# Performance work log

Hardware: AMD Instinct MI355X
Metric: run time of the kernel (lower is better)

Reference implementation:

```python
import jax, jax.numpy as jnp
import numpy as np

B, T, I, H, O = 1024, 512, 1, 64, 1


def _lstm_layer(x, Wih, Whh, bih, bhh):
    # x: [B,T,in]; Wih: [4H,in]; Whh: [4H,H]; biases: [4H]
    # Precompute input contribution for all timesteps (PyTorch adds both biases).
    xg = jnp.einsum('bti,gi->btg', x, Wih) + bih + bhh  # [B,T,4H]
    h0 = jnp.zeros((x.shape[0], H), x.dtype)

    def step(carry, xg_t):
        h, c = carry
        gates = xg_t + h @ Whh.T  # [B,4H], torch gate order i,f,g,o
        i, f, g, o = jnp.split(gates, 4, axis=-1)
        c = jax.nn.sigmoid(f) * c + jax.nn.sigmoid(i) * jnp.tanh(g)
        h = jax.nn.sigmoid(o) * jnp.tanh(c)
        return (h, c), h

    (_, _), hs = jax.lax.scan(step, (h0, h0), jnp.swapaxes(xg, 0, 1))
    return jnp.swapaxes(hs, 0, 1)  # [B,T,H]


def setup_inputs() -> dict:
    key = jax.random.key(0)
    ks = jax.random.split(key, 12)
    s = 1.0 / np.sqrt(H)  # torch LSTM/Linear init scale
    u = lambda k, shp: jax.random.uniform(k, shp, jnp.float32, -s, s)
    return {
        'x': jax.random.normal(ks[0], (B, T, I), jnp.float32),
        'W_ih0': u(ks[1], (4 * H, I)), 'W_hh0': u(ks[2], (4 * H, H)),
        'b_ih0': u(ks[3], (4 * H,)), 'b_hh0': u(ks[4], (4 * H,)),
        'W_ih1': u(ks[5], (4 * H, H)), 'W_hh1': u(ks[6], (4 * H, H)),
        'b_ih1': u(ks[7], (4 * H,)), 'b_hh1': u(ks[8], (4 * H,)),
        'W_fc': u(ks[9], (O, H)), 'b_fc': u(ks[10], (O,)),
    }


def reference(x, W_ih0, W_hh0, b_ih0, b_hh0, W_ih1, W_hh1, b_ih1, b_hh1, W_fc, b_fc):
    h1 = _lstm_layer(x, W_ih0, W_hh0, b_ih0, b_hh0)   # layer 0
    h2 = _lstm_layer(h1, W_ih1, W_hh1, b_ih1, b_hh1)  # layer 1
    return h2[:, -1, :] @ W_fc.T + b_fc  # [B,O]
```

## Files before the change

### kernel.cpp

```cpp
#include <hip/hip_runtime.h>

#define BB 1024
#define TT 512
#define HH 64
#define NB 4
#define NTHR 512

typedef _Float16 half8 __attribute__((ext_vector_type(8)));
typedef float f32x4 __attribute__((ext_vector_type(4)));

#if defined(__has_builtin)
#  if __has_builtin(__builtin_amdgcn_rcpf)
#    define FRCP(v) __builtin_amdgcn_rcpf(v)
#  endif
#endif
#ifndef FRCP
#  define FRCP(v) (1.0f / (v))
#endif

#define MFMA16(A, B, C) __builtin_amdgcn_mfma_f32_16x16x32_f16((A), (B), (C), 0, 0, 0)

__device__ __forceinline__ float fsig(float v) {
    return FRCP(1.0f + __expf(-v));
}
__device__ __forceinline__ float ftanh(float v) {
    return fmaf(2.0f, fsig(2.0f * v), -1.0f);
}

__device__ __forceinline__ half8 load_frag(const float* __restrict__ W, int row, int k0) {
    const float4* p = (const float4*)(W + row * HH + k0);
    float4 u = p[0], v = p[1];
    half8 r;
    r[0] = (_Float16)u.x; r[1] = (_Float16)u.y; r[2] = (_Float16)u.z; r[3] = (_Float16)u.w;
    r[4] = (_Float16)v.x; r[5] = (_Float16)v.y; r[6] = (_Float16)v.z; r[7] = (_Float16)v.w;
    return r;
}

__global__ __launch_bounds__(NTHR, 2)
void lstm_mfma2(const float* __restrict__ x,
                const float* __restrict__ Wih0,
                const float* __restrict__ Whh0,
                const float* __restrict__ bih0,
                const float* __restrict__ bhh0,
                const float* __restrict__ Wih1,
                const float* __restrict__ Whh1,
                const float* __restrict__ bih1,
                const float* __restrict__ bhh1,
                const float* __restrict__ Wfc,
                const float* __restrict__ bfc,
                float* __restrict__ out)
{
    __shared__ float s_x[NB][TT + 1];
    __shared__ __align__(16) _Float16 s_h0b[2][NB][80];
    __shared__ __align__(16) _Float16 s_h1b[2][NB][80];

    const int t    = threadIdx.x;
    const int lane = t & 63;
    const int w    = t >> 6;
    const int b0   = blockIdx.x * NB;

    const int arow = lane & 15;
    const int g4   = lane >> 4;
    const int bsrc = lane & 3;

    const int rep   = (lane >> 2) & 3;
    const int layer = rep >> 1;
    const int dd    = rep & 1;
    const int u     = 8 * w + 4 * dd + g4;

    half8 a0[2][2], a1i[2][2], a1h[2][2];
#pragma unroll
    for (int d = 0; d < 2; ++d) {
        const int row = (arow & 3) * 64 + 8 * w + 4 * d + (arow >> 2);
#pragma unroll
        for (int kk = 0; kk < 2; ++kk) {
            const int k0 = kk * 32 + g4 * 8;
            a0[d][kk]  = load_frag(Whh0, row, k0);
            a1i[d][kk] = load_frag(Wih1, row, k0);
            a1h[d][kk] = load_frag(Whh1, row, k0);
        }
    }

    f32x4 cb0[2], cb1[2];
#pragma unroll
    for (int d = 0; d < 2; ++d) {
        const int uu = 8 * w + 4 * d + g4;
#pragma unroll
        for (int q = 0; q < 4; ++q) {
            const int r = q * 64 + uu;
            cb0[d][q] = bih0[r] + bhh0[r];
            cb1[d][q] = bih1[r] + bhh1[r];
        }
    }
    float xw[4];
#pragma unroll
    for (int q = 0; q < 4; ++q) {
        xw[q] = (layer == 0) ? Wih0[q * 64 + u] : 0.0f;
    }

#pragma unroll
    for (int k = 0; k < (NB * TT) / NTHR; ++k) {
        int idx = t + NTHR * k;
        int nb  = idx >> 9;
        int pos = idx & (TT - 1);
        s_x[nb][pos] = x[(b0 + nb) * TT + pos];
    }
    {
        _Float16* z0 = &s_h0b[0][0][0];
        _Float16* z1 = &s_h1b[0][0][0];
        for (int i = t; i < 2 * NB * 80; i += NTHR) {
            z0[i] = (_Float16)0.0f;
            z1[i] = (_Float16)0.0f;
        }
    }

    float cst = 0.0f;
    __syncthreads();

    for (int s = 0; s <= TT; ++s) {
        const int rb = s & 1;
        const int wb = rb ^ 1;
        const int xs = (s < TT) ? s : (TT - 1);
        const float xv = s_x[bsrc][xs];

        const _Float16* h0p = &s_h0b[rb][bsrc][g4 * 8];
        const _Float16* h1p = &s_h1b[rb][bsrc][g4 * 8];
        half8 bh0_0 = *(const half8*)(h0p);
        half8 bh0_1 = *(const half8*)(h0p + 32);
        half8 bh1_0 = *(const half8*)(h1p);
        half8 bh1_1 = *(const half8*)(h1p + 32);

        f32x4 c0_0 = cb0[0], c0_1 = cb0[1];
        c0_0 = MFMA16(a0[0][0], bh0_0, c0_0);
        c0_1 = MFMA16(a0[1][0], bh0_0, c0_1);
        c0_0 = MFMA16(a0[0][1], bh0_1, c0_0);
        c0_1 = MFMA16(a0[1][1], bh0_1, c0_1);
        f32x4 c1a0 = cb1[0], c1a1 = cb1[1];
        f32x4 c1b0 = {0.f, 0.f, 0.f, 0.f}, c1b1 = {0.f, 0.f, 0.f, 0.f};
        c1a0 = MFMA16(a1i[0][0], bh0_0, c1a0);
        c1a1 = MFMA16(a1i[1][0], bh0_0, c1a1);
        c1b0 = MFMA16(a1h[0][0], bh1_0, c1b0);
        c1b1 = MFMA16(a1h[1][0], bh1_0, c1b1);
        c1a0 = MFMA16(a1i[0][1], bh0_1, c1a0);
        c1a1 = MFMA16(a1i[1][1], bh0_1, c1a1);
        c1b0 = MFMA16(a1h[0][1], bh1_1, c1b0);
        c1b1 = MFMA16(a1h[1][1], bh1_1, c1b1);
        f32x4 c1_0 = c1a0 + c1b0;
        f32x4 c1_1 = c1a1 + c1b1;

        f32x4 t0 = dd ? c0_1 : c0_0;
        f32x4 t1 = dd ? c1_1 : c1_0;
        f32x4 gv = layer ? t1 : t0;

        float gi = fmaf(xw[0], xv, gv[0]);
        float gf = fmaf(xw[1], xv, gv[1]);
        float gg = fmaf(xw[2], xv, gv[2]);
        float go = fmaf(xw[3], xv, gv[3]);

        const bool active = layer ? (s >= 1) : (s < TT);
        if (active) {
            float i_ = fsig(gi);
            float f_ = fsig(gf);
            float g_ = ftanh(gg);
            float o_ = fsig(go);
            cst = fmaf(f_, cst, i_ * g_);
            float hn = o_ * ftanh(cst);
            _Float16* dst = layer ? &s_h1b[wb][bsrc][u] : &s_h0b[wb][bsrc][u];
            *dst = (_Float16)hn;
        }
        __syncthreads();
    }

    if (t < NB * HH) {
        const int nb = t >> 6;
        const int j  = t & 63;
        float v = (float)s_h1b[1][nb][j] * Wfc[j];
#pragma unroll
        for (int off = 32; off > 0; off >>= 1) {
            v += __shfl_down(v, off);
        }
        if (j == 0) out[b0 + nb] = v + bfc[0];
    }
}

extern "C" void kernel_launch(void* const* d_in, const int* in_sizes, int n_in,
                              void* d_out, int out_size, void* d_ws, size_t ws_size,
                              hipStream_t stream) {
    const float* x    = (const float*)d_in[0];
    const float* Wih0 = (const float*)d_in[1];
    const float* Whh0 = (const float*)d_in[2];
    const float* bih0 = (const float*)d_in[3];
    const float* bhh0 = (const float*)d_in[4];
    const float* Wih1 = (const float*)d_in[5];
    const float* Whh1 = (const float*)d_in[6];
    const float* bih1 = (const float*)d_in[7];
    const float* bhh1 = (const float*)d_in[8];
    const float* Wfc  = (const float*)d_in[9];
    const float* bfc  = (const float*)d_in[10];
    float* out = (float*)d_out;

    lstm_mfma2<<<dim3(BB / NB), dim3(NTHR), 0, stream>>>(
        x, Wih0, Whh0, bih0, bhh0, Wih1, Whh1, bih1, bhh1, Wfc, bfc, out);
}
```

Measured before the change: 317.7 us.

## Halve batch per block and use four waves each covering 16 hidden units

Each block now handles 2 batch rows with 4 waves instead of 4 rows with 8 waves, so each wave owns 16 hidden units and issues 4 MFMA tiles per gate group. Lane mapping changes so each lane picks its gate value from 8 replicas (layer × dtile) over 2 batch sources. The launch has twice as many blocks, and each per-step barrier syncs only 4 waves, which is meant to cut barrier cost and raise parallelism across CUs. In exchange each wave does twice the MFMA work, holds twice the weight registers, and does more redundant selection work. The h buffers are padded to 96 halves.

```diff
diff --git a/kernel.cpp b/kernel.cpp
--- a/kernel.cpp
+++ b/kernel.cpp
@@ -3,8 +3,9 @@
 #define BB 1024
 #define TT 512
 #define HH 64
-#define NB 4
-#define NTHR 512
+#define NB 2
+#define NTHR 256
+#define HPAD 96
 
 typedef _Float16 half8 __attribute__((ext_vector_type(8)));
 typedef float f32x4 __attribute__((ext_vector_type(4)));
@@ -37,7 +38,7 @@
 }
 
 __global__ __launch_bounds__(NTHR, 2)
-void lstm_mfma2(const float* __restrict__ x,
+void lstm_mfma3(const float* __restrict__ x,
                 const float* __restrict__ Wih0,
                 const float* __restrict__ Whh0,
                 const float* __restrict__ bih0,
@@ -51,8 +52,8 @@
                 float* __restrict__ out)
 {
     __shared__ float s_x[NB][TT + 1];
-    __shared__ __align__(16) _Float16 s_h0b[2][NB][80];
-    __shared__ __align__(16) _Float16 s_h1b[2][NB][80];
+    __shared__ __align__(16) _Float16 s_h0b[2][NB][HPAD];
+    __shared__ __align__(16) _Float16 s_h1b[2][NB][HPAD];
 
     const int t    = threadIdx.x;
     const int lane = t & 63;
@@ -61,17 +62,16 @@
 
     const int arow = lane & 15;
     const int g4   = lane >> 4;
-    const int bsrc = lane & 3;
-
-    const int rep   = (lane >> 2) & 3;
-    const int layer = rep >> 1;
-    const int dd    = rep & 1;
-    const int u     = 8 * w + 4 * dd + g4;
-
-    half8 a0[2][2], a1i[2][2], a1h[2][2];
-#pragma unroll
-    for (int d = 0; d < 2; ++d) {
-        const int row = (arow & 3) * 64 + 8 * w + 4 * d + (arow >> 2);
+    const int bsrc = lane & 1;
+    const int rep   = (lane >> 1) & 7;
+    const int layer = rep & 1;
+    const int dtile = rep >> 1;
+    const int u     = 16 * w + 4 * dtile + g4;
+
+    half8 a0[4][2], a1i[4][2], a1h[4][2];
+#pragma unroll
+    for (int d = 0; d < 4; ++d) {
+        const int row = (arow & 3) * 64 + 16 * w + 4 * d + (arow >> 2);
 #pragma unroll
         for (int kk = 0; kk < 2; ++kk) {
             const int k0 = kk * 32 + g4 * 8;
@@ -81,10 +81,10 @@
         }
     }
 
-    f32x4 cb0[2], cb1[2];
-#pragma unroll
-    for (int d = 0; d < 2; ++d) {
-        const int uu = 8 * w + 4 * d + g4;
+    f32x4 cb0[4], cb1[4];
+#pragma unroll
+    for (int d = 0; d < 4; ++d) {
+        const int uu = 16 * w + 4 * d + g4;
 #pragma unroll
         for (int q = 0; q < 4; ++q) {
             const int r = q * 64 + uu;
@@ -108,7 +108,7 @@
     {
         _Float16* z0 = &s_h0b[0][0][0];
         _Float16* z1 = &s_h1b[0][0][0];
-        for (int i = t; i < 2 * NB * 80; i += NTHR) {
+        for (int i = t; i < 2 * NB * HPAD; i += NTHR) {
             z0[i] = (_Float16)0.0f;
             z1[i] = (_Float16)0.0f;
         }
@@ -130,26 +130,32 @@
         half8 bh1_0 = *(const half8*)(h1p);
         half8 bh1_1 = *(const half8*)(h1p + 32);
 
-        f32x4 c0_0 = cb0[0], c0_1 = cb0[1];
-        c0_0 = MFMA16(a0[0][0], bh0_0, c0_0);
-        c0_1 = MFMA16(a0[1][0], bh0_0, c0_1);
-        c0_0 = MFMA16(a0[0][1], bh0_1, c0_0);
-        c0_1 = MFMA16(a0[1][1], bh0_1, c0_1);
-        f32x4 c1a0 = cb1[0], c1a1 = cb1[1];
-        f32x4 c1b0 = {0.f, 0.f, 0.f, 0.f}, c1b1 = {0.f, 0.f, 0.f, 0.f};
-        c1a0 = MFMA16(a1i[0][0], bh0_0, c1a0);
-        c1a1 = MFMA16(a1i[1][0], bh0_0, c1a1);
-        c1b0 = MFMA16(a1h[0][0], bh1_0, c1b0);
-        c1b1 = MFMA16(a1h[1][0], bh1_0, c1b1);
-        c1a0 = MFMA16(a1i[0][1], bh0_1, c1a0);
-        c1a1 = MFMA16(a1i[1][1], bh0_1, c1a1);
-        c1b0 = MFMA16(a1h[0][1], bh1_1, c1b0);
-        c1b1 = MFMA16(a1h[1][1], bh1_1, c1b1);
-        f32x4 c1_0 = c1a0 + c1b0;
-        f32x4 c1_1 = c1a1 + c1b1;
-
-        f32x4 t0 = dd ? c0_1 : c0_0;
-        f32x4 t1 = dd ? c1_1 : c1_0;
+        f32x4 c0[4], c1[4];
+#pragma unroll
+        for (int d = 0; d < 4; ++d) c0[d] = cb0[d];
+#pragma unroll
+        for (int d = 0; d < 4; ++d) c0[d] = MFMA16(a0[d][0], bh0_0, c0[d]);
+#pragma unroll
+        for (int d = 0; d < 4; ++d) c0[d] = MFMA16(a0[d][1], bh0_1, c0[d]);
+#pragma unroll
+        for (int d = 0; d < 4; ++d) c1[d] = cb1[d];
+#pragma unroll
+        for (int d = 0; d < 4; ++d) c1[d] = MFMA16(a1i[d][0], bh0_0, c1[d]);
+#pragma unroll
+        for (int d = 0; d < 4; ++d) c1[d] = MFMA16(a1i[d][1], bh0_1, c1[d]);
+#pragma unroll
+        for (int d = 0; d < 4; ++d) c1[d] = MFMA16(a1h[d][0], bh1_0, c1[d]);
+#pragma unroll
+        for (int d = 0; d < 4; ++d) c1[d] = MFMA16(a1h[d][1], bh1_1, c1[d]);
+
+        const bool d1 = (dtile & 1) != 0;
+        const bool d2 = (dtile & 2) != 0;
+        f32x4 ta = d1 ? c0[1] : c0[0];
+        f32x4 tb = d1 ? c0[3] : c0[2];
+        f32x4 t0 = d2 ? tb : ta;
+        f32x4 ua = d1 ? c1[1] : c1[0];
+        f32x4 ub = d1 ? c1[3] : c1[2];
+        f32x4 t1 = d2 ? ub : ua;
         f32x4 gv = layer ? t1 : t0;
 
         float gi = fmaf(xw[0], xv, gv[0]);
@@ -199,6 +205,6 @@
     const float* bfc  = (const float*)d_in[10];
     float* out = (float*)d_out;
 
-    lstm_mfma2<<<dim3(BB / NB), dim3(NTHR), 0, stream>>>(
+    lstm_mfma3<<<dim3(BB / NB), dim3(NTHR), 0, stream>>>(
         x, Wih0, Whh0, bih0, bhh0, Wih1, Whh1, bih1, bhh1, Wfc, bfc, out);
 }
```

Result: slower. 386.1 us (+21.5%).

## Split hidden units across 16 waves to halve per-wave MFMA chain per step

Applied to the files above, without the earlier changes.

Doubles the block to 1024 threads so each wave owns 4 hidden units instead of 8. Each wave's per-step MFMA count drops from 12 to 6, and its A-fragment register footprint halves. The intent is to shorten the serial recurrence critical path per timestep. In exchange, the barrier now synchronises 16 waves instead of 8, half the lanes sit idle during the activation math, and per-CU occupancy in blocks may change.

```diff
diff --git a/kernel.cpp b/kernel.cpp
--- a/kernel.cpp
+++ b/kernel.cpp
@@ -4,7 +4,7 @@
 #define TT 512
 #define HH 64
 #define NB 4
-#define NTHR 512
+#define NTHR 1024
 
 typedef _Float16 half8 __attribute__((ext_vector_type(8)));
 typedef float f32x4 __attribute__((ext_vector_type(4)));
@@ -36,8 +36,8 @@
     return r;
 }
 
-__global__ __launch_bounds__(NTHR, 2)
-void lstm_mfma2(const float* __restrict__ x,
+__global__ __launch_bounds__(NTHR, 4)
+void lstm_mfma6(const float* __restrict__ x,
                 const float* __restrict__ Wih0,
                 const float* __restrict__ Whh0,
                 const float* __restrict__ bih0,
@@ -62,35 +62,29 @@
     const int arow = lane & 15;
     const int g4   = lane >> 4;
     const int bsrc = lane & 3;
+    const int rep    = (lane >> 2) & 3;
+    const int layer  = rep & 1;
+    const int actrep = ((rep >> 1) == 0);
+    const int u      = 4 * w + g4;
 
-    const int rep   = (lane >> 2) & 3;
-    const int layer = rep >> 1;
-    const int dd    = rep & 1;
-    const int u     = 8 * w + 4 * dd + g4;
-
-    half8 a0[2][2], a1i[2][2], a1h[2][2];
-#pragma unroll
-    for (int d = 0; d < 2; ++d) {
-        const int row = (arow & 3) * 64 + 8 * w + 4 * d + (arow >> 2);
+    half8 a0[2], a1i[2], a1h[2];
+    {
+        const int row = (arow & 3) * 64 + 4 * w + (arow >> 2);
 #pragma unroll
         for (int kk = 0; kk < 2; ++kk) {
             const int k0 = kk * 32 + g4 * 8;
-            a0[d][kk]  = load_frag(Whh0, row, k0);
-            a1i[d][kk] = load_frag(Wih1, row, k0);
-            a1h[d][kk] = load_frag(Whh1, row, k0);
+            a0[kk]  = load_frag(Whh0, row, k0);
+            a1i[kk] = load_frag(Wih1, row, k0);
+            a1h[kk] = load_frag(Whh1, row, k0);
         }
     }
 
-    f32x4 cb0[2], cb1[2];
+    f32x4 cb0, cb1;
 #pragma unroll
-    for (int d = 0; d < 2; ++d) {
-        const int uu = 8 * w + 4 * d + g4;
-#pragma unroll
-        for (int q = 0; q < 4; ++q) {
-            const int r = q * 64 + uu;
-            cb0[d][q] = bih0[r] + bhh0[r];
-            cb1[d][q] = bih1[r] + bhh1[r];
-        }
+    for (int q = 0; q < 4; ++q) {
+        const int r = q * 64 + u;
+        cb0[q] = bih0[r] + bhh0[r];
+        cb1[q] = bih1[r] + bhh1[r];
     }
     float xw[4];
 #pragma unroll
@@ -105,13 +99,9 @@
         int pos = idx & (TT - 1);
         s_x[nb][pos] = x[(b0 + nb) * TT + pos];
     }
-    {
-        _Float16* z0 = &s_h0b[0][0][0];
-        _Float16* z1 = &s_h1b[0][0][0];
-        for (int i = t; i < 2 * NB * 80; i += NTHR) {
-            z0[i] = (_Float16)0.0f;
-            z1[i] = (_Float16)0.0f;
-        }
+    if (t < 2 * NB * 80) {
+        (&s_h0b[0][0][0])[t] = (_Float16)0.0f;
+        (&s_h1b[0][0][0])[t] = (_Float16)0.0f;
     }
 
     float cst = 0.0f;
@@ -130,35 +120,26 @@
         half8 bh1_0 = *(const half8*)(h1p);
         half8 bh1_1 = *(const half8*)(h1p + 32);
 
-        f32x4 c0_0 = cb0[0], c0_1 = cb0[1];
-        c0_0 = MFMA16(a0[0][0], bh0_0, c0_0);
-        c0_1 = MFMA16(a0[1][0], bh0_0, c0_1);
-        c0_0 = MFMA16(a0[0][1], bh0_1, c0_0);
-        c0_1 = MFMA16(a0[1][1], bh0_1, c0_1);
-        f32x4 c1a0 = cb1[0], c1a1 = cb1[1];
-        f32x4 c1b0 = {0.f, 0.f, 0.f, 0.f}, c1b1 = {0.f, 0.f, 0.f, 0.f};
-        c1a0 = MFMA16(a1i[0][0], bh0_0, c1a0);
-        c1a1 = MFMA16(a1i[1][0], bh0_0, c1a1);
-        c1b0 = MFMA16(a1h[0][0], bh1_0, c1b0);
-        c1b1 = MFMA16(a1h[1][0], bh1_0, c1b1);
-        c1a0 = MFMA16(a1i[0][1], bh0_1, c1a0);
-        c1a1 = MFMA16(a1i[1][1], bh0_1, c1a1);
-        c1b0 = MFMA16(a1h[0][1], bh1_1, c1b0);
-        c1b1 = MFMA16(a1h[1][1], bh1_1, c1b1);
-        f32x4 c1_0 = c1a0 + c1b0;
-        f32x4 c1_1 = c1a1 + c1b1;
+        f32x4 c0 = cb0;
+        c0 = MFMA16(a0[0], bh0_0, c0);
+        c0 = MFMA16(a0[1], bh0_1, c0);
+        f32x4 c1a = cb1;
+        f32x4 c1b = {0.f, 0.f, 0.f, 0.f};
+        c1a = MFMA16(a1i[0], bh0_0, c1a);
+        c1b = MFMA16(a1h[0], bh1_0, c1b);
+        c1a = MFMA16(a1i[1], bh0_1, c1a);
+        c1b = MFMA16(a1h[1], bh1_1, c1b);
+        f32x4 c1 = c1a + c1b;
 
-        f32x4 t0 = dd ? c0_1 : c0_0;
-        f32x4 t1 = dd ? c1_1 : c1_0;
-        f32x4 gv = layer ? t1 : t0;
+        f32x4 gv = layer ? c1 : c0;
 
         float gi = fmaf(xw[0], xv, gv[0]);
         float gf = fmaf(xw[1], xv, gv[1]);
         float gg = fmaf(xw[2], xv, gv[2]);
         float go = fmaf(xw[3], xv, gv[3]);
 
-        const bool active = layer ? (s >= 1) : (s < TT);
-        if (active) {
+        const bool act = actrep && (layer ? (s >= 1) : (s < TT));
+        if (act) {
             float i_ = fsig(gi);
             float f_ = fsig(gf);
             float g_ = ftanh(gg);
@@ -199,6 +180,6 @@
     const float* bfc  = (const float*)d_in[10];
     float* out = (float*)d_out;
 
-    lstm_mfma2<<<dim3(BB / NB), dim3(NTHR), 0, stream>>>(
+    lstm_mfma6<<<dim3(BB / NB), dim3(NTHR), 0, stream>>>(
         x, Wih0, Whh0, bih0, bhh0, Wih1, Whh1, bih1, bhh1, Wfc, bfc, out);
 }
```

Result: slower. 374.4 us (+17.8%).
